# Performance work log

Measured on AMD Instinct MI355X. Metric: run time of the kernel, lower is better.

The kernel has to match this reference:

```python
import jax, jax.numpy as jnp
import numpy as np

N = 50000      # nodes
E = 1600000    # edges (avg degree 32)
F_IN = 128
F_OUT = 64
ALPHA = 0.2    # LeakyReLU negative slope


def setup_inputs() -> dict:
    key = jax.random.key(0)
    ks = jax.random.split(key, 11)
    xav = 1.414 * (2.0 / (F_IN + F_OUT)) ** 0.5  # xavier_normal gain=1.414
    xav_a = 1.414 * (2.0 / (1 + 2 * F_OUT)) ** 0.5
    return {
        "input": jax.random.normal(ks[0], (N, F_IN), jnp.float32),
        "p_h": jax.random.normal(ks[1], (N, F_IN), jnp.float32),
        "new_h": jax.random.normal(ks[2], (N, F_IN), jnp.float32),
        "edge": jax.random.randint(ks[3], (2, E), 0, N),
        "edge_col": jax.random.randint(ks[4], (2, N), 0, N),
        "row_i": jax.random.randint(ks[5], (N,), 0, N),
        "row_resort": jax.random.randint(ks[6], (E,), 0, N),
        "adj": jnp.zeros((1,), jnp.float32),  # unused by forward (kept for signature parity)
        "W": jax.random.normal(ks[7], (F_IN, F_OUT), jnp.float32) * xav,
        "a1": jax.random.normal(ks[8], (1, 2 * F_OUT), jnp.float32) * xav_a,
        "a2": jax.random.normal(ks[9], (1, 2 * F_OUT), jnp.float32) * xav_a,
    }


def segment_softmax(src, index, num_segments):
    # torch_geometric.utils.softmax: numerically-stable softmax grouped by index
    m = jax.ops.segment_max(src, index, num_segments=num_segments)
    m = jnp.where(jnp.isfinite(m), m, 0.0)  # empty segments -> 0
    ex = jnp.exp(src - m[index])
    s = jax.ops.segment_sum(ex, index, num_segments=num_segments)
    return ex / (s[index] + 1e-16)


def reference(input, p_h, new_h, edge, edge_col, row_i, row_resort, adj, W, a1, a2):
    n = input.shape[0]
    fo = W.shape[1]
    h = input @ W            # [N, Fo]
    ph = p_h @ W             # [N, Fo]
    nh = new_h @ W           # [N, Fo]

    # a1 @ cat(h_src, p_h).T  ==  h_src @ a1_left + p_h @ a1_right  (avoids [E,2Fo] concat)
    a1l, a1r = a1[0, :fo], a1[0, fo:]
    col_score = h[edge_col[0]] @ a1l + ph @ a1r                 # [N]
    edge_col_e = jnp.exp(-jax.nn.leaky_relu(col_score, ALPHA))
    edge_col_e = segment_softmax(edge_col_e, row_i, n)

    a2l, a2r = a2[0, :fo], a2[0, fo:]
    row_score = nh[row_resort] @ a2l + h[edge[1]] @ a2r          # [E]
    edge_row_e = jnp.exp(-jax.nn.leaky_relu(row_score, ALPHA))

    edge_e = edge_row_e * edge_col_e[row_resort]                 # [E]

    # special_spmm(edge, edge_e, [N,N], ones) == segment row-sum
    e_rowsum = jax.ops.segment_sum(edge_e, edge[0], num_segments=n)[:, None]  # [N,1]
    e_rowsum = e_rowsum + jnp.where(e_rowsum == 0, 1.0, 0.0)

    attention_e = edge_e[:, None] / e_rowsum[edge[0]]            # [E,1]

    # dropout p=0.0 (eval): identity
    # special_spmm(edge, edge_e, [N,N], h) == segment-weighted aggregate
    h_prime = jax.ops.segment_sum(edge_e[:, None] * h[edge[1]], edge[0], num_segments=n)
    h_prime = h_prime / e_rowsum

    return jax.nn.elu(h_prime), edge, attention_e
```

## Files before the change

### kernel.cpp

```cpp
#include <hip/hip_runtime.h>

#define NN 50000
#define NE 1600000
#define FIN 128
#define FOUT 64
#define ALPHA 0.2f

#define RANGE 256
#define NB 196
#define EPB 2048
#define NBLK 782

typedef float v2f __attribute__((ext_vector_type(2)));

__device__ inline int ldi(const void* p, size_t i, int isi64) {
    int v = isi64 ? (int)((const long long*)p)[i] : ((const int*)p)[i];
    return v < 0 ? 0 : (v >= NN ? NN - 1 : v);
}

__device__ inline unsigned short f2bf(float x) {
    unsigned u = __float_as_uint(x);
    return (unsigned short)((u + 0x7FFFu + ((u >> 16) & 1u)) >> 16);
}

__device__ inline v2f bfu2(unsigned u) {
    v2f r;
    r.x = __uint_as_float(u << 16);
    r.y = __uint_as_float(u & 0xFFFF0000u);
    return r;
}

__global__ __launch_bounds__(256) void k_su(const int* __restrict__ edge32, int* __restrict__ iflag,
                                            const float* __restrict__ W, const float* __restrict__ a1,
                                            const float* __restrict__ a2, float* __restrict__ u) {
    if (blockIdx.x == 0) {
        __shared__ int zodd;
        if (threadIdx.x == 0) zodd = 0;
        __syncthreads();
        int z = 0;
        for (int i = threadIdx.x; i < 2048; i += 256)
            if (edge32[2 * i + 1] == 0) z++;
        atomicAdd(&zodd, z);
        __syncthreads();
        if (threadIdx.x == 0) *iflag = (zodd > 2000) ? 1 : 0;
    } else {
        int k = threadIdx.x;
        if (k < FIN) {
            float u1 = 0.f, u2 = 0.f, u3 = 0.f, u4 = 0.f;
            for (int j = 0; j < FOUT; j++) {
                float w = W[k * FOUT + j];
                u1 += w * a1[j];
                u2 += w * a1[FOUT + j];
                u3 += w * a2[j];
                u4 += w * a2[FOUT + j];
            }
            u[k] = u1; u[128 + k] = u2; u[256 + k] = u3; u[384 + k] = u4;
        }
    }
}

__global__ __launch_bounds__(256) void k_gemm(const float* __restrict__ X,
                                              const float* __restrict__ W,
                                              unsigned short* __restrict__ h) {
    __shared__ float wlds[FIN * FOUT];
    __shared__ float xlds[4][4][FIN];
    int tid = threadIdx.x;
    for (int i = tid; i < FIN * FOUT; i += 256) wlds[i] = W[i];
    int wave = tid >> 6, lane = tid & 63;
    int base = blockIdx.x * 16 + wave * 4;
    for (int n0 = 0; n0 < 4; n0++) {
        float2 b = ((const float2*)(X + (size_t)(base + n0) * FIN))[lane];
        xlds[wave][n0][2 * lane] = b.x;
        xlds[wave][n0][2 * lane + 1] = b.y;
    }
    __syncthreads();
    float a0 = 0.f, a1v = 0.f, a2v = 0.f, a3 = 0.f;
    for (int k = 0; k < FIN; k++) {
        float w = wlds[k * FOUT + lane];
        a0  += xlds[wave][0][k] * w;
        a1v += xlds[wave][1][k] * w;
        a2v += xlds[wave][2][k] * w;
        a3  += xlds[wave][3][k] * w;
    }
    h[(size_t)(base + 0) * FOUT + lane] = f2bf(a0);
    h[(size_t)(base + 1) * FOUT + lane] = f2bf(a1v);
    h[(size_t)(base + 2) * FOUT + lane] = f2bf(a2v);
    h[(size_t)(base + 3) * FOUT + lane] = f2bf(a3);
}

__global__ __launch_bounds__(256) void k_svec_cnt(const float* __restrict__ input,
                                                  const float* __restrict__ p_h,
                                                  const float* __restrict__ new_h,
                                                  const float* __restrict__ u,
                                                  float* __restrict__ s1, float* __restrict__ s2,
                                                  float* __restrict__ sc ,
                                                  float* __restrict__ s4,
                                                  const void* __restrict__ edge,
                                                  const int* __restrict__ iflag,
                                                  int* __restrict__ cntm) {
    __shared__ int hist[NB];
    int tid = threadIdx.x;
    if (blockIdx.x < 12500) {
        int lane = tid & 63;
        int v = blockIdx.x * 4 + (tid >> 6);
        size_t row = (size_t)v * FIN;
        float2 bi = ((const float2*)(input + row))[lane];
        float2 bp = ((const float2*)(p_h   + row))[lane];
        float2 bn = ((const float2*)(new_h + row))[lane];
        float p1 = bi.x * u[2 * lane]       + bi.y * u[2 * lane + 1];
        float p2 = bp.x * u[128 + 2 * lane] + bp.y * u[128 + 2 * lane + 1];
        float p3 = bn.x * u[256 + 2 * lane] + bn.y * u[256 + 2 * lane + 1];
        float p4 = bi.x * u[384 + 2 * lane] + bi.y * u[384 + 2 * lane + 1];
#pragma unroll
        for (int off = 32; off > 0; off >>= 1) {
            p1 += __shfl_down(p1, off, 64);
            p2 += __shfl_down(p2, off, 64);
            p3 += __shfl_down(p3, off, 64);
            p4 += __shfl_down(p4, off, 64);
        }
        if (lane == 0) { s1[v] = p1; s2[v] = p2; sc[2 * v] = p3; s4[v] = p4; }
    } else {
        int cb = blockIdx.x - 12500;
        for (int t = tid; t < NB; t += 256) hist[t] = 0;
        __syncthreads();
        int i64 = *iflag;
        int base = cb * EPB;
        int b0[8]; bool act[8];
#pragma unroll
        for (int k = 0; k < 8; k++) {
            int e = base + k * 256 + tid;
            act[k] = e < NE;
            b0[k] = ldi(edge, act[k] ? e : NE - 1, i64) >> 8;
        }
#pragma unroll
        for (int k = 0; k < 8; k++)
            if (act[k]) atomicAdd(&hist[b0[k]], 1);
        __syncthreads();
        for (int t = tid; t < NB; t += 256)
            cntm[cb * NB + t] = hist[t];
    }
}

__global__ void k_colscore(const float* __restrict__ s1, const float* __restrict__ s2,
                           const void* __restrict__ edge_col, const void* __restrict__ row_i,
                           const int* __restrict__ iflag,
                           float* __restrict__ ec, unsigned int* __restrict__ m) {
    int i = blockIdx.x * 256 + threadIdx.x;
    if (i >= NN) return;
    int i64 = *iflag;
    float cs = s1[ldi(edge_col, i, i64)] + s2[i];
    float l = cs > 0.f ? cs : ALPHA * cs;
    float e = expf(-l);
    ec[i] = e;
    atomicMax(&m[ldi(row_i, i, i64)], __float_as_uint(e));
}

__global__ void k_expsum(float* __restrict__ ec, const unsigned int* __restrict__ m,
                         const void* __restrict__ row_i, const int* __restrict__ iflag,
                         float* __restrict__ ssum) {
    int i = blockIdx.x * 256 + threadIdx.x;
    if (i >= NN) return;
    int r = ldi(row_i, i, *iflag);
    float e = expf(ec[i] - __uint_as_float(m[r]));
    ec[i] = e;
    atomicAdd(&ssum[r], e);
}

__global__ void k_norm(const float* __restrict__ ex, const float* __restrict__ ssum,
                       const void* __restrict__ row_i, const int* __restrict__ iflag,
                       float* __restrict__ sc ) {
    int i = blockIdx.x * 256 + threadIdx.x;
    if (i >= NN) return;
    sc[2 * i + 1] = ex[i] / (ssum[ldi(row_i, i, *iflag)] + 1e-16f);
}

__global__ __launch_bounds__(1024) void k_colscan(const int* __restrict__ cntm,
                                                  int* __restrict__ colpre,
                                                  int* __restrict__ bcnt) {
    __shared__ int s[1024];
    int b = blockIdx.x, tid = threadIdx.x;
    int x = (tid < NBLK) ? cntm[(size_t)tid * NB + b] : 0;
    s[tid] = x;
    __syncthreads();
    for (int off = 1; off < 1024; off <<= 1) {
        int t = (tid >= off) ? s[tid - off] : 0;
        __syncthreads();
        s[tid] += t;
        __syncthreads();
    }
    if (tid < NBLK) colpre[(size_t)tid * NB + b] = s[tid] - x;
    if (tid == 1023) bcnt[b] = s[1023];
}

__global__ __launch_bounds__(256) void k_bscan(const int* __restrict__ bcnt,
                                               int* __restrict__ bstart,
                                               int* __restrict__ start) {
    __shared__ int s[256];
    int tid = threadIdx.x;
    int x = (tid < NB) ? bcnt[tid] : 0;
    s[tid] = x;
    __syncthreads();
    for (int off = 1; off < 256; off <<= 1) {
        int t = (tid >= off) ? s[tid - off] : 0;
        __syncthreads();
        s[tid] += t;
        __syncthreads();
    }
    if (tid < NB) bstart[tid] = s[tid] - x;
    if (tid == 0) { bstart[NB] = NE; start[NN] = NE; }
}

__global__ __launch_bounds__(512) void k_edgeA(const float2* __restrict__ sc, const float* __restrict__ s4,
                                               const void* __restrict__ edge, const void* __restrict__ row_resort,
                                               const int* __restrict__ iflag,
                                               const int* __restrict__ bstart, const int* __restrict__ colpre,
                                               uint2* __restrict__ tmp,
                                               float* __restrict__ edge_e ) {
    __shared__ int hist[NB];
    __shared__ int bbase[NB];
    int tid = threadIdx.x;
    for (int t = tid; t < NB; t += 512) {
        hist[t] = 0;
        bbase[t] = bstart[t] + colpre[(size_t)blockIdx.x * NB + t];
    }
    __syncthreads();
    int i64 = *iflag;
    int base = blockIdx.x * EPB;
    int e0[4], e1[4], rr[4]; bool act[4];
#pragma unroll
    for (int k = 0; k < 4; k++) {
        int e = base + k * 512 + tid;
        act[k] = e < NE;
        size_t ec = act[k] ? (size_t)e : (size_t)(NE - 1);
        e0[k] = ldi(edge, ec, i64);
        e1[k] = ldi(edge, (size_t)NE + ec, i64);
        rr[k] = ldi(row_resort, ec, i64);
    }
    float2 c[4]; float s4v[4];
#pragma unroll
    for (int k = 0; k < 4; k++) {
        c[k] = sc[rr[k]];
        s4v[k] = s4[e1[k]];
    }
    unsigned key[4]; float val[4]; int rk[4], bk[4];
#pragma unroll
    for (int k = 0; k < 4; k++) {
        float rsv = c[k].x + s4v[k];
        float l = rsv > 0.f ? rsv : ALPHA * rsv;
        float ee = expf(-l) * c[k].y;
        if (act[k]) edge_e[base + k * 512 + tid] = ee;
        key[k] = (unsigned)e0[k] | ((unsigned)e1[k] << 16);
        val[k] = ee;
        bk[k] = e0[k] >> 8;
        rk[k] = act[k] ? atomicAdd(&hist[bk[k]], 1) : 0;
    }
#pragma unroll
    for (int k = 0; k < 4; k++)
        if (act[k])
            tmp[bbase[bk[k]] + rk[k]] = make_uint2(key[k], __float_as_uint(val[k]));
}

__global__ __launch_bounds__(512) void k_edgeB(const uint2* __restrict__ tmp,
                                               const int* __restrict__ bstart,
                                               int* __restrict__ start,
                                               float2* __restrict__ pairs) {
    __shared__ int cnt[RANGE];
    __shared__ int s[RANGE];
    __shared__ int cur[RANGE];
    int b = blockIdx.x;
    int tid = threadIdx.x;
    int v0 = b * RANGE;
    if (tid < RANGE) cnt[tid] = 0;
    __syncthreads();
    int lo = bstart[b], hi = bstart[b + 1];
    for (int i = lo + tid; i < hi; i += 512)
        atomicAdd(&cnt[tmp[i].x & 0xFFu], 1);
    __syncthreads();
    if (tid < RANGE) s[tid] = cnt[tid];
    __syncthreads();
    for (int off = 1; off < RANGE; off <<= 1) {
        int t = 0;
        if (tid < RANGE && tid >= off) t = s[tid - off];
        __syncthreads();
        if (tid < RANGE) s[tid] += t;
        __syncthreads();
    }
    if (tid < RANGE) {
        int g = lo + s[tid] - cnt[tid];
        cur[tid] = g;
        int v = v0 + tid;
        if (v < NN) start[v] = g;
    }
    __syncthreads();
    for (int i = lo + tid; i < hi; i += 512) {
        uint2 r = tmp[i];
        int pos = atomicAdd(&cur[r.x & 0xFFu], 1);
        pairs[pos] = make_float2(__int_as_float((int)(r.x >> 16)), __uint_as_float(r.y));
    }
}

__global__ __launch_bounds__(512) void k_agg(const unsigned short* __restrict__ h,
                                             const float2* __restrict__ pairs,
                                             const int* __restrict__ start,
                                             float* __restrict__ ersum,
                                             float* __restrict__ out0) {
    int lane = threadIdx.x & 63;
    int q  = lane >> 3;
    int fq = lane & 7;
    int v = blockIdx.x * 8 + (threadIdx.x >> 6);
    int a = start[v], b = start[v + 1];
    v2f a01 = {0.f, 0.f}, a23 = {0.f, 0.f}, a45 = {0.f, 0.f}, a67 = {0.f, 0.f};
    float rs = 0.f;
    int bfull = a + ((b - a) & ~15);
    int j = a;
    for (; j < bfull; j += 16) {
        float2 pA = pairs[j + q];
        float2 pB = pairs[j + 8 + q];
        uint4 hA = *(const uint4*)(h + (((size_t)__float_as_int(pA.x)) << 6) + 8 * fq);
        uint4 hB = *(const uint4*)(h + (((size_t)__float_as_int(pB.x)) << 6) + 8 * fq);
        v2f eA = {pA.y, pA.y}, eB = {pB.y, pB.y};
        a01 += eA * bfu2(hA.x);
        a23 += eA * bfu2(hA.y);
        a45 += eA * bfu2(hA.z);
        a67 += eA * bfu2(hA.w);
        a01 += eB * bfu2(hB.x);
        a23 += eB * bfu2(hB.y);
        a45 += eB * bfu2(hB.z);
        a67 += eB * bfu2(hB.w);
        rs += pA.y + pB.y;
    }
    if (j < b) {
        int eAi = j + q, eBi = j + 8 + q;
        float2 pA = (eAi < b) ? pairs[eAi] : make_float2(__int_as_float(0), 0.f);
        float2 pB = (eBi < b) ? pairs[eBi] : make_float2(__int_as_float(0), 0.f);
        uint4 hA = *(const uint4*)(h + (((size_t)__float_as_int(pA.x)) << 6) + 8 * fq);
        uint4 hB = *(const uint4*)(h + (((size_t)__float_as_int(pB.x)) << 6) + 8 * fq);
        v2f eA = {pA.y, pA.y}, eB = {pB.y, pB.y};
        a01 += eA * bfu2(hA.x);
        a23 += eA * bfu2(hA.y);
        a45 += eA * bfu2(hA.z);
        a67 += eA * bfu2(hA.w);
        a01 += eB * bfu2(hB.x);
        a23 += eB * bfu2(hB.y);
        a45 += eB * bfu2(hB.z);
        a67 += eB * bfu2(hB.w);
        rs += pA.y + pB.y;
    }
#pragma unroll
    for (int off = 8; off <= 32; off <<= 1) {
        v2f t01, t23, t45, t67;
        t01.x = __shfl_xor(a01.x, off, 64); t01.y = __shfl_xor(a01.y, off, 64);
        t23.x = __shfl_xor(a23.x, off, 64); t23.y = __shfl_xor(a23.y, off, 64);
        t45.x = __shfl_xor(a45.x, off, 64); t45.y = __shfl_xor(a45.y, off, 64);
        t67.x = __shfl_xor(a67.x, off, 64); t67.y = __shfl_xor(a67.y, off, 64);
        a01 += t01; a23 += t23; a45 += t45; a67 += t67;
        rs  += __shfl_xor(rs, off, 64);
    }
    v2f ap = (q >> 1) == 0 ? a01 : (q >> 1) == 1 ? a23 : (q >> 1) == 2 ? a45 : a67;
    float av = (q & 1) ? ap.y : ap.x;
    rs += (rs == 0.f) ? 1.f : 0.f;
    float ev = av / rs;
    ev = ev > 0.f ? ev : expm1f(ev);
    out0[(size_t)v * FOUT + 8 * fq + q] = ev;
    if (lane == 0) ersum[v] = rs;
}

__global__ __launch_bounds__(256) void k_final(const void* __restrict__ edge, const int* __restrict__ iflag,
                                               const float* __restrict__ ersum,
                                               float* __restrict__ out2, float* __restrict__ out1) {
    int i = blockIdx.x * 256 + threadIdx.x;
    int i64 = *iflag;
    int v = i64 ? (int)((const long long*)edge)[i] : ((const int*)edge)[i];
    out1[i] = (float)v;
    if (i < NE) {
        int e0 = v < 0 ? 0 : (v >= NN ? NN - 1 : v);
        out2[i] = out2[i] / ersum[e0];
    }
}

extern "C" void kernel_launch(void* const* d_in, const int* in_sizes, int n_in,
                              void* d_out, int out_size, void* d_ws, size_t ws_size,
                              hipStream_t stream) {
    int ix[3] = {0, 1, 2}; int nx = 0;
    int iE = 3, iCol = 4, iRowI = 5, iRes = 6, iW = 8, iA1 = 9, iA2 = 10;
    bool a1seen = false;
    for (int i = 0; i < n_in; i++) {
        int s = in_sizes[i];
        if (s == NN * FIN) { if (nx < 3) ix[nx++] = i; }
        else if (s == 2 * NE) iE = i;
        else if (s == 2 * NN) iCol = i;
        else if (s == NN) iRowI = i;
        else if (s == NE) iRes = i;
        else if (s == FIN * FOUT) iW = i;
        else if (s == 2 * FOUT) { if (!a1seen) { iA1 = i; a1seen = true; } else iA2 = i; }
    }
    const float* input = (const float*)d_in[ix[0]];
    const float* p_h   = (const float*)d_in[ix[1]];
    const float* new_h = (const float*)d_in[ix[2]];
    const void* edge       = d_in[iE];
    const void* edge_col   = d_in[iCol];
    const void* row_i      = d_in[iRowI];
    const void* row_resort = d_in[iRes];
    const float* W  = (const float*)d_in[iW];
    const float* a1 = (const float*)d_in[iA1];
    const float* a2 = (const float*)d_in[iA2];

    float* out0 = (float*)d_out;
    float* out1 = out0 + (size_t)NN * FOUT;
    float* out2 = out1 + (size_t)2 * NE;

    uint2* tmp = (uint2*)out1;

    unsigned short* h = (unsigned short*)d_ws;
    float2* pairs  = (float2*)((float*)d_ws + (size_t)NN * FOUT);
    float*  s1     = (float*)(pairs + NE);
    float*  s2     = s1 + NN;
    float*  s4     = s2 + NN;
    float*  ec     = s4 + NN;
    float*  scf    = ec + NN;
    float*  mseg   = scf + 2 * (size_t)NN;
    float*  ssum   = mseg + NN;
    int*    bcnt   = (int*)(ssum + NN);
    int*    start  = bcnt + NB;
    int*    bstart = start + NN + 1;
    int*    cntm   = bstart + NB + 1;
    int*    colpre = cntm + (size_t)NBLK * NB;
    float*  ersum  = (float*)(colpre + (size_t)NBLK * NB);
    float*  u      = ersum + NN;
    int*    iflag  = (int*)(u + 512);

    hipMemsetAsync(mseg, 0, (size_t)2 * NN * sizeof(float), stream);

    k_su<<<2, 256, 0, stream>>>((const int*)edge, iflag, W, a1, a2, u);
    k_gemm<<<NN / 16, 256, 0, stream>>>(input, W, h);
    k_svec_cnt<<<12500 + NBLK, 256, 0, stream>>>(input, p_h, new_h, u, s1, s2, scf, s4,
                                                 edge, iflag, cntm);
    k_colscore<<<(NN + 255) / 256, 256, 0, stream>>>(s1, s2, edge_col, row_i, iflag, ec, (unsigned int*)mseg);
    k_expsum<<<(NN + 255) / 256, 256, 0, stream>>>(ec, (const unsigned int*)mseg, row_i, iflag, ssum);
    k_norm<<<(NN + 255) / 256, 256, 0, stream>>>(ec, ssum, row_i, iflag, scf);
    k_colscan<<<NB, 1024, 0, stream>>>(cntm, colpre, bcnt);
    k_bscan<<<1, 256, 0, stream>>>(bcnt, bstart, start);
    k_edgeA<<<NBLK, 512, 0, stream>>>((const float2*)scf, s4, edge, row_resort, iflag, bstart, colpre, tmp, out2);
    k_edgeB<<<NB, 512, 0, stream>>>(tmp, bstart, start, pairs);
    k_agg<<<NN / 8, 512, 0, stream>>>(h, pairs, start, ersum, out0);
    k_final<<<2 * NE / 256, 256, 0, stream>>>(edge, iflag, ersum, out2, out1);
}
```

Baseline: 280.5 us.

## Fuse local row sort into aggregation using LDS staging with 64-node buckets

Shrinks the bucket range from 256 to 64 nodes, giving 782 buckets, and fuses the per-bucket counting sort with the weighted aggregation in one kernel. Sorted (src, weight) pairs are staged in shared memory (up to 4096 entries) instead of being written to a global pairs array and read back, which removes one kernel launch and a global round trip. Buckets that do not fit fall back to a global spill buffer. The trade-offs are a larger column histogram and prefix-scan workload (782 buckets per block) and one block of 512 threads per 64 nodes, where each wave processes 8 nodes serially.

```diff
diff --git a/kernel.cpp b/kernel.cpp
--- a/kernel.cpp
+++ b/kernel.cpp
@@ -6,8 +6,9 @@
 #define FOUT 64
 #define ALPHA 0.2f
 
-#define RANGE 256
-#define NB 196
+#define RANGE 64
+#define NBK 782
+#define CAP 4096
 #define EPB 2048
 #define NBLK 782
 
@@ -98,7 +99,7 @@
                                                   const void* __restrict__ edge,
                                                   const int* __restrict__ iflag,
                                                   int* __restrict__ cntm) {
-    __shared__ int hist[NB];
+    __shared__ int hist[NBK];
     int tid = threadIdx.x;
     if (blockIdx.x < 12500) {
         int lane = tid & 63;
@@ -121,7 +122,7 @@
         if (lane == 0) { s1[v] = p1; s2[v] = p2; sc[2 * v] = p3; s4[v] = p4; }
     } else {
         int cb = blockIdx.x - 12500;
-        for (int t = tid; t < NB; t += 256) hist[t] = 0;
+        for (int t = tid; t < NBK; t += 256) hist[t] = 0;
         __syncthreads();
         int i64 = *iflag;
         int base = cb * EPB;
@@ -130,14 +131,14 @@
         for (int k = 0; k < 8; k++) {
             int e = base + k * 256 + tid;
             act[k] = e < NE;
-            b0[k] = ldi(edge, act[k] ? e : NE - 1, i64) >> 8;
+            b0[k] = ldi(edge, act[k] ? e : NE - 1, i64) >> 6;
         }
 #pragma unroll
         for (int k = 0; k < 8; k++)
             if (act[k]) atomicAdd(&hist[b0[k]], 1);
         __syncthreads();
-        for (int t = tid; t < NB; t += 256)
-            cntm[cb * NB + t] = hist[t];
+        for (int t = tid; t < NBK; t += 256)
+            cntm[(size_t)cb * NBK + t] = hist[t];
     }
 }
 
@@ -179,7 +180,7 @@
                                                   int* __restrict__ bcnt) {
     __shared__ int s[1024];
     int b = blockIdx.x, tid = threadIdx.x;
-    int x = (tid < NBLK) ? cntm[(size_t)tid * NB + b] : 0;
+    int x = (tid < NBLK) ? cntm[(size_t)tid * NBK + b] : 0;
     s[tid] = x;
     __syncthreads();
     for (int off = 1; off < 1024; off <<= 1) {
@@ -188,26 +189,25 @@
         s[tid] += t;
         __syncthreads();
     }
-    if (tid < NBLK) colpre[(size_t)tid * NB + b] = s[tid] - x;
+    if (tid < NBLK) colpre[(size_t)tid * NBK + b] = s[tid] - x;
     if (tid == 1023) bcnt[b] = s[1023];
 }
 
-__global__ __launch_bounds__(256) void k_bscan(const int* __restrict__ bcnt,
-                                               int* __restrict__ bstart,
-                                               int* __restrict__ start) {
-    __shared__ int s[256];
+__global__ __launch_bounds__(1024) void k_bscan(const int* __restrict__ bcnt,
+                                                int* __restrict__ bstart) {
+    __shared__ int s[1024];
     int tid = threadIdx.x;
-    int x = (tid < NB) ? bcnt[tid] : 0;
+    int x = (tid < NBK) ? bcnt[tid] : 0;
     s[tid] = x;
     __syncthreads();
-    for (int off = 1; off < 256; off <<= 1) {
+    for (int off = 1; off < 1024; off <<= 1) {
         int t = (tid >= off) ? s[tid - off] : 0;
         __syncthreads();
         s[tid] += t;
         __syncthreads();
     }
-    if (tid < NB) bstart[tid] = s[tid] - x;
-    if (tid == 0) { bstart[NB] = NE; start[NN] = NE; }
+    if (tid < NBK) bstart[tid] = s[tid] - x;
+    if (tid == 0) bstart[NBK] = NE;
 }
 
 __global__ __launch_bounds__(512) void k_edgeA(const float2* __restrict__ sc, const float* __restrict__ s4,
@@ -216,12 +216,12 @@
                                                const int* __restrict__ bstart, const int* __restrict__ colpre,
                                                uint2* __restrict__ tmp,
                                                float* __restrict__ edge_e ) {
-    __shared__ int hist[NB];
-    __shared__ int bbase[NB];
+    __shared__ int hist[NBK];
+    __shared__ int bbase[NBK];
     int tid = threadIdx.x;
-    for (int t = tid; t < NB; t += 512) {
+    for (int t = tid; t < NBK; t += 512) {
         hist[t] = 0;
-        bbase[t] = bstart[t] + colpre[(size_t)blockIdx.x * NB + t];
+        bbase[t] = bstart[t] + colpre[(size_t)blockIdx.x * NBK + t];
     }
     __syncthreads();
     int i64 = *iflag;
@@ -251,7 +251,7 @@
         if (act[k]) edge_e[base + k * 512 + tid] = ee;
         key[k] = (unsigned)e0[k] | ((unsigned)e1[k] << 16);
         val[k] = ee;
-        bk[k] = e0[k] >> 8;
+        bk[k] = e0[k] >> 6;
         rk[k] = act[k] ? atomicAdd(&hist[bk[k]], 1) : 0;
     }
 #pragma unroll
@@ -260,109 +260,125 @@
             tmp[bbase[bk[k]] + rk[k]] = make_uint2(key[k], __float_as_uint(val[k]));
 }
 
-__global__ __launch_bounds__(512) void k_edgeB(const uint2* __restrict__ tmp,
-                                               const int* __restrict__ bstart,
-                                               int* __restrict__ start,
-                                               float2* __restrict__ pairs) {
+__global__ __launch_bounds__(512) void k_aggB(const unsigned short* __restrict__ h,
+                                              const uint2* __restrict__ tmp,
+                                              const int* __restrict__ bstart,
+                                              uint2* __restrict__ spill,
+                                              float* __restrict__ ersum,
+                                              float* __restrict__ out0) {
+    __shared__ uint2 lp[CAP];
     __shared__ int cnt[RANGE];
-    __shared__ int s[RANGE];
+    __shared__ int bs[RANGE];
     __shared__ int cur[RANGE];
+    int tid = threadIdx.x;
     int b = blockIdx.x;
-    int tid = threadIdx.x;
     int v0 = b * RANGE;
     if (tid < RANGE) cnt[tid] = 0;
     __syncthreads();
     int lo = bstart[b], hi = bstart[b + 1];
+    int sz = hi - lo;
     for (int i = lo + tid; i < hi; i += 512)
-        atomicAdd(&cnt[tmp[i].x & 0xFFu], 1);
-    __syncthreads();
-    if (tid < RANGE) s[tid] = cnt[tid];
+        atomicAdd(&cnt[tmp[i].x & (RANGE - 1)], 1);
+    __syncthreads();
+    if (tid < RANGE) bs[tid] = cnt[tid];
     __syncthreads();
     for (int off = 1; off < RANGE; off <<= 1) {
         int t = 0;
-        if (tid < RANGE && tid >= off) t = s[tid - off];
-        __syncthreads();
-        if (tid < RANGE) s[tid] += t;
+        if (tid < RANGE && tid >= off) t = bs[tid - off];
+        __syncthreads();
+        if (tid < RANGE) bs[tid] += t;
         __syncthreads();
     }
     if (tid < RANGE) {
-        int g = lo + s[tid] - cnt[tid];
+        int g = bs[tid] - cnt[tid];
+        bs[tid] = g;
         cur[tid] = g;
-        int v = v0 + tid;
-        if (v < NN) start[v] = g;
-    }
-    __syncthreads();
-    for (int i = lo + tid; i < hi; i += 512) {
-        uint2 r = tmp[i];
-        int pos = atomicAdd(&cur[r.x & 0xFFu], 1);
-        pairs[pos] = make_float2(__int_as_float((int)(r.x >> 16)), __uint_as_float(r.y));
-    }
-}
-
-__global__ __launch_bounds__(512) void k_agg(const unsigned short* __restrict__ h,
-                                             const float2* __restrict__ pairs,
-                                             const int* __restrict__ start,
-                                             float* __restrict__ ersum,
-                                             float* __restrict__ out0) {
-    int lane = threadIdx.x & 63;
-    int q  = lane >> 3;
-    int fq = lane & 7;
-    int v = blockIdx.x * 8 + (threadIdx.x >> 6);
-    int a = start[v], b = start[v + 1];
-    v2f a01 = {0.f, 0.f}, a23 = {0.f, 0.f}, a45 = {0.f, 0.f}, a67 = {0.f, 0.f};
-    float rs = 0.f;
-    int bfull = a + ((b - a) & ~15);
-    int j = a;
-    for (; j < bfull; j += 16) {
-        float2 pA = pairs[j + q];
-        float2 pB = pairs[j + 8 + q];
-        uint4 hA = *(const uint4*)(h + (((size_t)__float_as_int(pA.x)) << 6) + 8 * fq);
-        uint4 hB = *(const uint4*)(h + (((size_t)__float_as_int(pB.x)) << 6) + 8 * fq);
-        v2f eA = {pA.y, pA.y}, eB = {pB.y, pB.y};
-        a01 += eA * bfu2(hA.x);
-        a23 += eA * bfu2(hA.y);
-        a45 += eA * bfu2(hA.z);
-        a67 += eA * bfu2(hA.w);
-        a01 += eB * bfu2(hB.x);
-        a23 += eB * bfu2(hB.y);
-        a45 += eB * bfu2(hB.z);
-        a67 += eB * bfu2(hB.w);
-        rs += pA.y + pB.y;
-    }
-    if (j < b) {
-        int eAi = j + q, eBi = j + 8 + q;
-        float2 pA = (eAi < b) ? pairs[eAi] : make_float2(__int_as_float(0), 0.f);
-        float2 pB = (eBi < b) ? pairs[eBi] : make_float2(__int_as_float(0), 0.f);
-        uint4 hA = *(const uint4*)(h + (((size_t)__float_as_int(pA.x)) << 6) + 8 * fq);
-        uint4 hB = *(const uint4*)(h + (((size_t)__float_as_int(pB.x)) << 6) + 8 * fq);
-        v2f eA = {pA.y, pA.y}, eB = {pB.y, pB.y};
-        a01 += eA * bfu2(hA.x);
-        a23 += eA * bfu2(hA.y);
-        a45 += eA * bfu2(hA.z);
-        a67 += eA * bfu2(hA.w);
-        a01 += eB * bfu2(hB.x);
-        a23 += eB * bfu2(hB.y);
-        a45 += eB * bfu2(hB.z);
-        a67 += eB * bfu2(hB.w);
-        rs += pA.y + pB.y;
-    }
-#pragma unroll
-    for (int off = 8; off <= 32; off <<= 1) {
-        v2f t01, t23, t45, t67;
-        t01.x = __shfl_xor(a01.x, off, 64); t01.y = __shfl_xor(a01.y, off, 64);
-        t23.x = __shfl_xor(a23.x, off, 64); t23.y = __shfl_xor(a23.y, off, 64);
-        t45.x = __shfl_xor(a45.x, off, 64); t45.y = __shfl_xor(a45.y, off, 64);
-        t67.x = __shfl_xor(a67.x, off, 64); t67.y = __shfl_xor(a67.y, off, 64);
-        a01 += t01; a23 += t23; a45 += t45; a67 += t67;
-        rs  += __shfl_xor(rs, off, 64);
-    }
-    v2f ap = (q >> 1) == 0 ? a01 : (q >> 1) == 1 ? a23 : (q >> 1) == 2 ? a45 : a67;
-    float av = (q & 1) ? ap.y : ap.x;
-    rs += (rs == 0.f) ? 1.f : 0.f;
-    float ev = av / rs;
-    ev = ev > 0.f ? ev : expm1f(ev);
-    out0[(size_t)v * FOUT + 8 * fq + q] = ev;
-    if (lane == 0) ersum[v] = rs;
+    }
+    __syncthreads();
+    bool inl = sz <= CAP;
+    if (inl) {
+        for (int i = lo + tid; i < hi; i += 512) {
+            uint2 r = tmp[i];
+            int pos = atomicAdd(&cur[r.x & (RANGE - 1)], 1);
+            lp[pos] = make_uint2(r.x >> 16, r.y);
+        }
+    } else {
+        for (int i = lo + tid; i < hi; i += 512) {
+            uint2 r = tmp[i];
+            int pos = atomicAdd(&cur[r.x & (RANGE - 1)], 1);
+            spill[lo + pos] = make_uint2(r.x >> 16, r.y);
+        }
+    }
+    __syncthreads();
+    const uint2* src = inl ? (const uint2*)lp : (spill + lo);
+    int lane = tid & 63, wid = tid >> 6;
+    int q = lane >> 3, fq = lane & 7;
+    for (int nn = 0; nn < 8; nn++) {
+        int n = wid * 8 + nn;
+        int a = bs[n];
+        int bnd = a + cnt[n];
+        v2f a01 = {0.f, 0.f}, a23 = {0.f, 0.f}, a45 = {0.f, 0.f}, a67 = {0.f, 0.f};
+        float rs = 0.f;
+        int bfull = a + ((bnd - a) & ~15);
+        int j = a;
+        for (; j < bfull; j += 16) {
+            uint2 pA = src[j + q];
+            uint2 pB = src[j + 8 + q];
+            float eeA = __uint_as_float(pA.y), eeB = __uint_as_float(pB.y);
+            uint4 hA = *(const uint4*)(h + (((size_t)pA.x) << 6) + 8 * fq);
+            uint4 hB = *(const uint4*)(h + (((size_t)pB.x) << 6) + 8 * fq);
+            v2f eA = {eeA, eeA}, eB = {eeB, eeB};
+            a01 += eA * bfu2(hA.x);
+            a23 += eA * bfu2(hA.y);
+            a45 += eA * bfu2(hA.z);
+            a67 += eA * bfu2(hA.w);
+            a01 += eB * bfu2(hB.x);
+            a23 += eB * bfu2(hB.y);
+            a45 += eB * bfu2(hB.z);
+            a67 += eB * bfu2(hB.w);
+            rs += eeA + eeB;
+        }
+        if (j < bnd) {
+            int iA = j + q, iB = j + 8 + q;
+            bool vA = iA < bnd, vB = iB < bnd;
+            uint2 pA = src[vA ? iA : a];
+            uint2 pB = src[vB ? iB : a];
+            float eeA = vA ? __uint_as_float(pA.y) : 0.f;
+            float eeB = vB ? __uint_as_float(pB.y) : 0.f;
+            uint4 hA = *(const uint4*)(h + (((size_t)pA.x) << 6) + 8 * fq);
+            uint4 hB = *(const uint4*)(h + (((size_t)pB.x) << 6) + 8 * fq);
+            v2f eA = {eeA, eeA}, eB = {eeB, eeB};
+            a01 += eA * bfu2(hA.x);
+            a23 += eA * bfu2(hA.y);
+            a45 += eA * bfu2(hA.z);
+            a67 += eA * bfu2(hA.w);
+            a01 += eB * bfu2(hB.x);
+            a23 += eB * bfu2(hB.y);
+            a45 += eB * bfu2(hB.z);
+            a67 += eB * bfu2(hB.w);
+            rs += eeA + eeB;
+        }
+#pragma unroll
+        for (int off = 8; off <= 32; off <<= 1) {
+            v2f t01, t23, t45, t67;
+            t01.x = __shfl_xor(a01.x, off, 64); t01.y = __shfl_xor(a01.y, off, 64);
+            t23.x = __shfl_xor(a23.x, off, 64); t23.y = __shfl_xor(a23.y, off, 64);
+            t45.x = __shfl_xor(a45.x, off, 64); t45.y = __shfl_xor(a45.y, off, 64);
+            t67.x = __shfl_xor(a67.x, off, 64); t67.y = __shfl_xor(a67.y, off, 64);
+            a01 += t01; a23 += t23; a45 += t45; a67 += t67;
+            rs  += __shfl_xor(rs, off, 64);
+        }
+        v2f ap = (q >> 1) == 0 ? a01 : (q >> 1) == 1 ? a23 : (q >> 1) == 2 ? a45 : a67;
+        float av = (q & 1) ? ap.y : ap.x;
+        rs += (rs == 0.f) ? 1.f : 0.f;
+        float ev = av / rs;
+        ev = ev > 0.f ? ev : expm1f(ev);
+        int v = v0 + n;
+        if (v < NN) {
+            out0[(size_t)v * FOUT + 8 * fq + q] = ev;
+            if (lane == 0) ersum[v] = rs;
+        }
+    }
 }
 
 __global__ __launch_bounds__(256) void k_final(const void* __restrict__ edge, const int* __restrict__ iflag,
@@ -412,8 +428,8 @@
     uint2* tmp = (uint2*)out1;
 
     unsigned short* h = (unsigned short*)d_ws;
-    float2* pairs  = (float2*)((float*)d_ws + (size_t)NN * FOUT);
-    float*  s1     = (float*)(pairs + NE);
+    uint2*  spill  = (uint2*)((float*)d_ws + (size_t)NN * FOUT);
+    float*  s1     = (float*)(spill + NE);
     float*  s2     = s1 + NN;
     float*  s4     = s2 + NN;
     float*  ec     = s4 + NN;
@@ -421,11 +437,10 @@
     float*  mseg   = scf + 2 * (size_t)NN;
     float*  ssum   = mseg + NN;
     int*    bcnt   = (int*)(ssum + NN);
-    int*    start  = bcnt + NB;
-    int*    bstart = start + NN + 1;
-    int*    cntm   = bstart + NB + 1;
-    int*    colpre = cntm + (size_t)NBLK * NB;
-    float*  ersum  = (float*)(colpre + (size_t)NBLK * NB);
+    int*    bstart = bcnt + NBK;
+    int*    cntm   = bstart + NBK + 1;
+    int*    colpre = cntm + (size_t)NBLK * NBK;
+    float*  ersum  = (float*)(colpre + (size_t)NBLK * NBK);
     float*  u      = ersum + NN;
     int*    iflag  = (int*)(u + 512);
 
@@ -438,10 +453,9 @@
     k_colscore<<<(NN + 255) / 256, 256, 0, stream>>>(s1, s2, edge_col, row_i, iflag, ec, (unsigned int*)mseg);
     k_expsum<<<(NN + 255) / 256, 256, 0, stream>>>(ec, (const unsigned int*)mseg, row_i, iflag, ssum);
     k_norm<<<(NN + 255) / 256, 256, 0, stream>>>(ec, ssum, row_i, iflag, scf);
-    k_colscan<<<NB, 1024, 0, stream>>>(cntm, colpre, bcnt);
-    k_bscan<<<1, 256, 0, stream>>>(bcnt, bstart, start);
+    k_colscan<<<NBK, 1024, 0, stream>>>(cntm, colpre, bcnt);
+    k_bscan<<<1, 1024, 0, stream>>>(bcnt, bstart);
     k_edgeA<<<NBLK, 512, 0, stream>>>((const float2*)scf, s4, edge, row_resort, iflag, bstart, colpre, tmp, out2);
-    k_edgeB<<<NB, 512, 0, stream>>>(tmp, bstart, start, pairs);
-    k_agg<<<NN / 8, 512, 0, stream>>>(h, pairs, start, ersum, out0);
+    k_aggB<<<NBK, 512, 0, stream>>>(h, tmp, bstart, spill, ersum, out0);
     k_final<<<2 * NE / 256, 256, 0, stream>>>(edge, iflag, ersum, out2, out1);
 }
```

New measurement: 283.4 us. No clear change (+1.0%).
